# Performance work log

Measured on AMD Instinct MI355X. Metric: run time of the kernel, lower is better.

## Reference

```python
import jax, jax.numpy as jnp
import numpy as np

D_K = 64
TAU = 1.0
THRESHOLD = 0.5


def setup_inputs() -> dict:
    key = jax.random.key(0)
    k1, k2, k3 = jax.random.split(key, 3)
    B, N, F = 32, 512, 320
    F_OBS = 256
    h = jax.random.normal(k1, (B, N, F), dtype=jnp.float32)
    # xavier_uniform with gain 1.414 on (F_OBS, D_K)
    limit = float(1.414 * np.sqrt(6.0 / (F_OBS + D_K)))
    a_link = jax.random.uniform(k2, (F_OBS, D_K), minval=-limit, maxval=limit, dtype=jnp.float32)
    b_link = jax.random.uniform(k3, (F_OBS, D_K), minval=-limit, maxval=limit, dtype=jnp.float32)
    return {"h": h, "a_link": a_link, "b_link": b_link, "rollout": 1}


def reference(h, a_link, b_link, rollout):
    F_OBS = a_link.shape[0]
    # original detaches the sliced features
    hx = jax.lax.stop_gradient(h[:, :, :F_OBS])
    h_i = jnp.einsum('bik,kl->bil', hx, a_link)
    h_j = jnp.einsum('bjk,kl->bjl', hx, b_link)
    logits = jnp.einsum('bil,bjl->bij', h_i, h_j) / jnp.sqrt(jnp.float32(D_K))

    # gumbel_sigmoid with rollout=True: no noise, just sigmoid(logits/tau)
    y_soft = jax.nn.sigmoid(logits / TAU)
    y_hard = (y_soft > THRESHOLD).astype(y_soft.dtype)
    # straight-through estimator
    A = y_hard - jax.lax.stop_gradient(y_soft) + y_soft

    B, N, _ = logits.shape
    eye_b = jnp.eye(N, dtype=bool)[None]          # [1, N, N]
    eye_f = jnp.eye(N, dtype=y_soft.dtype)[None]  # [1, N, N]

    # log-prob of the sampled hard edges, off-diagonal entries only
    sel = A * y_soft + (1.0 - A) * (1.0 - y_soft)
    logp = jnp.log(sel + 1e-8)
    probs = jnp.sum(jnp.where(eye_b, 0.0, logp), axis=(1, 2))  # [B]

    # zero the diagonal of A, then add identity (vectorized form of the per-batch diag loop)
    A_out = A - A * eye_f + eye_f
    # .squeeze(0) is a no-op for B > 1
    return A_out, probs
```

## Files before the change

### kernel.cpp

```cpp
#include <hip/hip_runtime.h>
#include <math.h>

#define BATCH   32
#define NPTS    512
#define FDIM    320
#define FOBS    256
#define DK      64
#define MROWS   (BATCH * NPTS)
#define A_ELEMS ((size_t)BATCH * NPTS * NPTS)

typedef __bf16  bf16x8 __attribute__((ext_vector_type(8)));
typedef float   f32x4  __attribute__((ext_vector_type(4)));
typedef ushort  u16x8  __attribute__((ext_vector_type(8)));
typedef ushort  u16x4  __attribute__((ext_vector_type(4)));

__device__ __forceinline__ ushort f2bf(float f) {
    unsigned u = __builtin_bit_cast(unsigned, f);
    return (ushort)((u + 0x7fffu + ((u >> 16) & 1u)) >> 16);
}

__device__ __forceinline__ bf16x8 ld_bf8(const ushort* p) {
    return __builtin_bit_cast(bf16x8, *reinterpret_cast<const uint4*>(p));
}

__global__ __launch_bounds__(256) void k0_wt(const float* __restrict__ al,
                                             const float* __restrict__ bl,
                                             ushort* __restrict__ wt) {
    const int n = blockIdx.x;
    const int k = threadIdx.x;
    const float* src = (n < 64) ? al : bl;
    const int nn = n & 63;
    wt[(size_t)n * FOBS + k] = f2bf(src[(size_t)k * DK + nn]);
}

__global__ __launch_bounds__(256) void k1_mfma(const float* __restrict__ h,
                                               const ushort* __restrict__ wt,
                                               ushort* __restrict__ hi,
                                               ushort* __restrict__ hj) {
    const int t  = threadIdx.x;
    const int w  = t >> 6;
    const int l  = t & 63;
    const int lr = l & 15;
    const int lg = l >> 4;
    const int rb = blockIdx.x * 32 + 16 * (w & 1);
    const int cb = 64 * (w >> 1);

    const float* hrow = h + (size_t)(rb + lr) * FDIM;
    bf16x8 bfr[8];
#pragma unroll
    for (int ks = 0; ks < 8; ++ks) {
        const float* p = hrow + ks * 32 + lg * 8;
        float4 v0 = *reinterpret_cast<const float4*>(p);
        float4 v1 = *reinterpret_cast<const float4*>(p + 4);
        u16x8 u;
        u[0] = f2bf(v0.x); u[1] = f2bf(v0.y); u[2] = f2bf(v0.z); u[3] = f2bf(v0.w);
        u[4] = f2bf(v1.x); u[5] = f2bf(v1.y); u[6] = f2bf(v1.z); u[7] = f2bf(v1.w);
        bfr[ks] = __builtin_bit_cast(bf16x8, u);
    }

    f32x4 acc[4];
#pragma unroll
    for (int cf = 0; cf < 4; ++cf) acc[cf] = (f32x4){0.f, 0.f, 0.f, 0.f};

#pragma unroll
    for (int ks = 0; ks < 8; ++ks) {
#pragma unroll
        for (int cf = 0; cf < 4; ++cf) {
            bf16x8 afr = ld_bf8(&wt[(size_t)(cb + 16 * cf + lr) * FOBS + ks * 32 + lg * 8]);
            acc[cf] = __builtin_amdgcn_mfma_f32_16x16x32_bf16(afr, bfr[ks], acc[cf], 0, 0, 0);
        }
    }

    ushort* dst = (cb == 0) ? hi : hj;
    const size_t m = (size_t)(rb + lr);
#pragma unroll
    for (int cf = 0; cf < 4; ++cf) {
        u16x4 v;
#pragma unroll
        for (int r = 0; r < 4; ++r) v[r] = f2bf(acc[cf][r]);
        *reinterpret_cast<u16x4*>(&dst[m * DK + 16 * cf + lg * 4]) = v;
    }
}

__global__ __launch_bounds__(256, 4) void k2_mfma(const ushort* __restrict__ hi,
                                                  const ushort* __restrict__ hj,
                                                  float* __restrict__ Aout,
                                                  float* __restrict__ partials) {
    __shared__ float red[4];
    const int id  = blockIdx.x;
    const int sub = id >> 3;
    const int b   = (id & 7) * 4 + (sub >> 6);
    const int it  = (sub >> 3) & 7;
    const int jt  = sub & 7;

    const int t  = threadIdx.x;
    const int w  = t >> 6;
    const int l  = t & 63;
    const int lr = l & 15;
    const int lg = l >> 4;
    const int i0 = it * 64, j0 = jt * 64;

    const ushort* hib = hi + ((size_t)b * NPTS + i0) * DK;
    const ushort* hjb = hj + ((size_t)b * NPTS + j0) * DK;

    bf16x8 afr[2];
#pragma unroll
    for (int ks = 0; ks < 2; ++ks)
        afr[ks] = ld_bf8(&hjb[(size_t)(16 * w + lr) * DK + ks * 32 + lg * 8]);

    bf16x8 bfr[4][2];
#pragma unroll
    for (int itt = 0; itt < 4; ++itt)
#pragma unroll
        for (int ks = 0; ks < 2; ++ks)
            bfr[itt][ks] = ld_bf8(&hib[(size_t)(16 * itt + lr) * DK + ks * 32 + lg * 8]);

    f32x4 acc[4];
#pragma unroll
    for (int itt = 0; itt < 4; ++itt) acc[itt] = (f32x4){0.f, 0.f, 0.f, 0.f};

#pragma unroll
    for (int ks = 0; ks < 2; ++ks)
#pragma unroll
        for (int itt = 0; itt < 4; ++itt)
            acc[itt] = __builtin_amdgcn_mfma_f32_16x16x32_bf16(
                afr[ks], bfr[itt][ks], acc[itt], 0, 0, 0);

    float lsum = 0.f;
    const int colbase = j0 + 16 * w + lg * 4;
#pragma unroll
    for (int itt = 0; itt < 4; ++itt) {
        const int row = i0 + 16 * itt + lr;
        f32x4 ov;
#pragma unroll
        for (int r = 0; r < 4; ++r) {
            float x  = acc[itt][r] * 0.125f;
            float ax = fabsf(x);
            float nl = __logf(1.0f + __expf(-ax));
            bool diag = (row == colbase + r);
            ov[r] = (diag || x > 0.f) ? 1.f : 0.f;
            if (!diag) lsum -= nl;
        }
        __builtin_nontemporal_store(ov,
            reinterpret_cast<f32x4*>(&Aout[((size_t)b * NPTS + row) * NPTS + colbase]));
    }

#pragma unroll
    for (int off = 32; off > 0; off >>= 1) lsum += __shfl_down(lsum, off);
    if (l == 0) red[w] = lsum;
    __syncthreads();
    if (t == 0) {
        float s = (red[0] + red[1]) + (red[2] + red[3]);
        partials[(size_t)b * 64 + it * 8 + jt] = s;
    }
}

__global__ __launch_bounds__(64) void k3_reduce(const float* __restrict__ partials,
                                                float* __restrict__ probs) {
    int b = blockIdx.x;
    float s = partials[(size_t)b * 64 + threadIdx.x];
#pragma unroll
    for (int off = 32; off > 0; off >>= 1) s += __shfl_down(s, off);
    if (threadIdx.x == 0) probs[b] = s;
}

extern "C" void kernel_launch(void* const* d_in, const int* in_sizes, int n_in,
                              void* d_out, int out_size, void* d_ws, size_t ws_size,
                              hipStream_t stream) {
    const float* h  = (const float*)d_in[0];
    const float* al = (const float*)d_in[1];
    const float* bl = (const float*)d_in[2];
    float* out = (float*)d_out;

    ushort* hi      = (ushort*)d_ws;
    ushort* hj      = hi + (size_t)MROWS * DK;
    ushort* wt      = hj + (size_t)MROWS * DK;
    float* partials = (float*)(wt + 128 * FOBS);

    k0_wt<<<128, 256, 0, stream>>>(al, bl, wt);

    k1_mfma<<<MROWS / 32, 256, 0, stream>>>(h, wt, hi, hj);

    k2_mfma<<<(NPTS / 64) * (NPTS / 64) * BATCH, 256, 0, stream>>>(
        hi, hj, out, partials);

    k3_reduce<<<BATCH, 64, 0, stream>>>(partials, out + A_ELEMS);
}
```

Before: 38.70 us.

## Fuse projection GEMM into pairwise logits kernel, recompute h_j per tile

Merges the projection kernel and the pairwise logits kernel into one kernel. Each block computes its 64 h_i rows into swizzled LDS, then for four 64-column j tiles recomputes h_j from h and rearranges the accumulator fragments into MFMA operands with lane shuffles. This removes the hi/hj round trip through global memory and one launch. In exchange, h_j projection work is redundantly recomputed 8 times per batch, and the grid shrinks to 512 blocks.

```diff
diff --git a/kernel.cpp b/kernel.cpp
--- a/kernel.cpp
+++ b/kernel.cpp
@@ -11,16 +11,25 @@
 
 typedef __bf16  bf16x8 __attribute__((ext_vector_type(8)));
 typedef float   f32x4  __attribute__((ext_vector_type(4)));
-typedef ushort  u16x8  __attribute__((ext_vector_type(8)));
 typedef ushort  u16x4  __attribute__((ext_vector_type(4)));
 
 __device__ __forceinline__ ushort f2bf(float f) {
     unsigned u = __builtin_bit_cast(unsigned, f);
     return (ushort)((u + 0x7fffu + ((u >> 16) & 1u)) >> 16);
 }
-
+__device__ __forceinline__ unsigned pbf2(float a, float b) {
+    return (unsigned)f2bf(a) | ((unsigned)f2bf(b) << 16);
+}
 __device__ __forceinline__ bf16x8 ld_bf8(const ushort* p) {
     return __builtin_bit_cast(bf16x8, *reinterpret_cast<const uint4*>(p));
+}
+__device__ __forceinline__ bf16x8 cvt8(const float* p) {
+    float4 v0 = *reinterpret_cast<const float4*>(p);
+    float4 v1 = *reinterpret_cast<const float4*>(p + 4);
+    uint4 u;
+    u.x = pbf2(v0.x, v0.y); u.y = pbf2(v0.z, v0.w);
+    u.z = pbf2(v1.x, v1.y); u.w = pbf2(v1.z, v1.w);
+    return __builtin_bit_cast(bf16x8, u);
 }
 
 __global__ __launch_bounds__(256) void k0_wt(const float* __restrict__ al,
@@ -33,116 +42,139 @@
     wt[(size_t)n * FOBS + k] = f2bf(src[(size_t)k * DK + nn]);
 }
 
-__global__ __launch_bounds__(256) void k1_mfma(const float* __restrict__ h,
-                                               const ushort* __restrict__ wt,
-                                               ushort* __restrict__ hi,
-                                               ushort* __restrict__ hj) {
+__global__ __launch_bounds__(256, 3) void kU(const float* __restrict__ h,
+                                             const ushort* __restrict__ wt,
+                                             float* __restrict__ Aout,
+                                             float* __restrict__ partials) {
+    __shared__ ushort hi_lds[64][72];
+    __shared__ float red[4];
+
+    const int id  = blockIdx.x;
+    const int sub = id >> 3;
+    const int b   = (id & 7) * 4 + (sub >> 4);
+    const int rem = sub & 15;
+    const int it  = rem >> 1, jh = rem & 1;
+    const int i0 = it * 64, jbase = jh * 256;
+
     const int t  = threadIdx.x;
     const int w  = t >> 6;
     const int l  = t & 63;
     const int lr = l & 15;
     const int lg = l >> 4;
-    const int rb = blockIdx.x * 32 + 16 * (w & 1);
-    const int cb = 64 * (w >> 1);
-
-    const float* hrow = h + (size_t)(rb + lr) * FDIM;
-    bf16x8 bfr[8];
-#pragma unroll
-    for (int ks = 0; ks < 8; ++ks) {
-        const float* p = hrow + ks * 32 + lg * 8;
-        float4 v0 = *reinterpret_cast<const float4*>(p);
-        float4 v1 = *reinterpret_cast<const float4*>(p + 4);
-        u16x8 u;
-        u[0] = f2bf(v0.x); u[1] = f2bf(v0.y); u[2] = f2bf(v0.z); u[3] = f2bf(v0.w);
-        u[4] = f2bf(v1.x); u[5] = f2bf(v1.y); u[6] = f2bf(v1.z); u[7] = f2bf(v1.w);
-        bfr[ks] = __builtin_bit_cast(bf16x8, u);
+
+    const float* hb = h + (size_t)b * NPTS * FDIM;
+
+    {
+        const float* hrow = hb + (size_t)(i0 + 16 * w + lr) * FDIM;
+        bf16x8 hfr[8];
+#pragma unroll
+        for (int ks = 0; ks < 8; ++ks) hfr[ks] = cvt8(hrow + ks * 32 + lg * 8);
+
+        f32x4 acc[4];
+#pragma unroll
+        for (int cf = 0; cf < 4; ++cf) acc[cf] = (f32x4){0.f, 0.f, 0.f, 0.f};
+#pragma unroll
+        for (int ks = 0; ks < 8; ++ks)
+#pragma unroll
+            for (int cf = 0; cf < 4; ++cf) {
+                bf16x8 afr = ld_bf8(&wt[(size_t)(16 * cf + lr) * FOBS + ks * 32 + lg * 8]);
+                acc[cf] = __builtin_amdgcn_mfma_f32_16x16x32_bf16(afr, hfr[ks], acc[cf], 0, 0, 0);
+            }
+        const int row = 16 * w + lr;
+        const int xr  = (row & 3) << 4;
+#pragma unroll
+        for (int cf = 0; cf < 4; ++cf) {
+            u16x4 v;
+#pragma unroll
+            for (int r = 0; r < 4; ++r) v[r] = f2bf(acc[cf][r]);
+            int colb = (32 * cf + 8 * lg) ^ xr;
+            *reinterpret_cast<u16x4*>(reinterpret_cast<char*>(&hi_lds[row][0]) + colb) = v;
+        }
     }
-
-    f32x4 acc[4];
-#pragma unroll
-    for (int cf = 0; cf < 4; ++cf) acc[cf] = (f32x4){0.f, 0.f, 0.f, 0.f};
-
-#pragma unroll
-    for (int ks = 0; ks < 8; ++ks) {
+    __syncthreads();
+
+    bf16x8 hifr[4][2];
+#pragma unroll
+    for (int itt = 0; itt < 4; ++itt)
+#pragma unroll
+        for (int ks = 0; ks < 2; ++ks) {
+            int row  = 16 * itt + lr;
+            int colb = (64 * ks + 16 * lg) ^ ((row & 3) << 4);
+            hifr[itt][ks] = *reinterpret_cast<bf16x8*>(
+                reinterpret_cast<char*>(&hi_lds[row][0]) + colb);
+        }
+
+    float lsum = 0.f;
+    const int s0 = lr + 16 * (2 * (lg & 1));
+    const int s1 = s0 + 16;
+    const bool hicf = (lg >> 1) != 0;
+
+    for (int jt = 0; jt < 4; ++jt) {
+        const int j0 = jbase + jt * 64;
+
+        f32x4 acc[4];
+#pragma unroll
+        for (int cf = 0; cf < 4; ++cf) acc[cf] = (f32x4){0.f, 0.f, 0.f, 0.f};
+        {
+            const float* hrow = hb + (size_t)(j0 + 16 * w + lr) * FDIM;
+#pragma unroll
+            for (int ks = 0; ks < 8; ++ks) {
+                bf16x8 hfr = cvt8(hrow + ks * 32 + lg * 8);
+#pragma unroll
+                for (int cf = 0; cf < 4; ++cf) {
+                    bf16x8 afr = ld_bf8(&wt[(size_t)(64 + 16 * cf + lr) * FOBS + ks * 32 + lg * 8]);
+                    acc[cf] = __builtin_amdgcn_mfma_f32_16x16x32_bf16(afr, hfr, acc[cf], 0, 0, 0);
+                }
+            }
+        }
+        unsigned dA[4], dB[4];
 #pragma unroll
         for (int cf = 0; cf < 4; ++cf) {
-            bf16x8 afr = ld_bf8(&wt[(size_t)(cb + 16 * cf + lr) * FOBS + ks * 32 + lg * 8]);
-            acc[cf] = __builtin_amdgcn_mfma_f32_16x16x32_bf16(afr, bfr[ks], acc[cf], 0, 0, 0);
-        }
-    }
-
-    ushort* dst = (cb == 0) ? hi : hj;
-    const size_t m = (size_t)(rb + lr);
-#pragma unroll
-    for (int cf = 0; cf < 4; ++cf) {
-        u16x4 v;
-#pragma unroll
-        for (int r = 0; r < 4; ++r) v[r] = f2bf(acc[cf][r]);
-        *reinterpret_cast<u16x4*>(&dst[m * DK + 16 * cf + lg * 4]) = v;
-    }
-}
-
-__global__ __launch_bounds__(256, 4) void k2_mfma(const ushort* __restrict__ hi,
-                                                  const ushort* __restrict__ hj,
-                                                  float* __restrict__ Aout,
-                                                  float* __restrict__ partials) {
-    __shared__ float red[4];
-    const int id  = blockIdx.x;
-    const int sub = id >> 3;
-    const int b   = (id & 7) * 4 + (sub >> 6);
-    const int it  = (sub >> 3) & 7;
-    const int jt  = sub & 7;
-
-    const int t  = threadIdx.x;
-    const int w  = t >> 6;
-    const int l  = t & 63;
-    const int lr = l & 15;
-    const int lg = l >> 4;
-    const int i0 = it * 64, j0 = jt * 64;
-
-    const ushort* hib = hi + ((size_t)b * NPTS + i0) * DK;
-    const ushort* hjb = hj + ((size_t)b * NPTS + j0) * DK;
-
-    bf16x8 afr[2];
-#pragma unroll
-    for (int ks = 0; ks < 2; ++ks)
-        afr[ks] = ld_bf8(&hjb[(size_t)(16 * w + lr) * DK + ks * 32 + lg * 8]);
-
-    bf16x8 bfr[4][2];
-#pragma unroll
-    for (int itt = 0; itt < 4; ++itt)
+            dA[cf] = pbf2(acc[cf][0], acc[cf][1]);
+            dB[cf] = pbf2(acc[cf][2], acc[cf][3]);
+        }
+        bf16x8 ajf[2];
+#pragma unroll
+        for (int ks = 0; ks < 2; ++ks) {
+            unsigned d0a = __shfl(dA[2 * ks],     s0), d0b = __shfl(dA[2 * ks + 1], s0);
+            unsigned d1a = __shfl(dB[2 * ks],     s0), d1b = __shfl(dB[2 * ks + 1], s0);
+            unsigned d2a = __shfl(dA[2 * ks],     s1), d2b = __shfl(dA[2 * ks + 1], s1);
+            unsigned d3a = __shfl(dB[2 * ks],     s1), d3b = __shfl(dB[2 * ks + 1], s1);
+            uint4 u;
+            u.x = hicf ? d0b : d0a;
+            u.y = hicf ? d1b : d1a;
+            u.z = hicf ? d2b : d2a;
+            u.w = hicf ? d3b : d3a;
+            ajf[ks] = __builtin_bit_cast(bf16x8, u);
+        }
+
+        f32x4 lac[4];
+#pragma unroll
+        for (int itt = 0; itt < 4; ++itt) lac[itt] = (f32x4){0.f, 0.f, 0.f, 0.f};
 #pragma unroll
         for (int ks = 0; ks < 2; ++ks)
-            bfr[itt][ks] = ld_bf8(&hib[(size_t)(16 * itt + lr) * DK + ks * 32 + lg * 8]);
-
-    f32x4 acc[4];
-#pragma unroll
-    for (int itt = 0; itt < 4; ++itt) acc[itt] = (f32x4){0.f, 0.f, 0.f, 0.f};
-
-#pragma unroll
-    for (int ks = 0; ks < 2; ++ks)
-#pragma unroll
-        for (int itt = 0; itt < 4; ++itt)
-            acc[itt] = __builtin_amdgcn_mfma_f32_16x16x32_bf16(
-                afr[ks], bfr[itt][ks], acc[itt], 0, 0, 0);
-
-    float lsum = 0.f;
-    const int colbase = j0 + 16 * w + lg * 4;
-#pragma unroll
-    for (int itt = 0; itt < 4; ++itt) {
-        const int row = i0 + 16 * itt + lr;
-        f32x4 ov;
-#pragma unroll
-        for (int r = 0; r < 4; ++r) {
-            float x  = acc[itt][r] * 0.125f;
-            float ax = fabsf(x);
-            float nl = __logf(1.0f + __expf(-ax));
-            bool diag = (row == colbase + r);
-            ov[r] = (diag || x > 0.f) ? 1.f : 0.f;
-            if (!diag) lsum -= nl;
-        }
-        __builtin_nontemporal_store(ov,
-            reinterpret_cast<f32x4*>(&Aout[((size_t)b * NPTS + row) * NPTS + colbase]));
+#pragma unroll
+            for (int itt = 0; itt < 4; ++itt)
+                lac[itt] = __builtin_amdgcn_mfma_f32_16x16x32_bf16(
+                    ajf[ks], hifr[itt][ks], lac[itt], 0, 0, 0);
+
+        const int colbase = j0 + 16 * w + 4 * lg;
+#pragma unroll
+        for (int itt = 0; itt < 4; ++itt) {
+            const int row = i0 + 16 * itt + lr;
+            f32x4 ov;
+#pragma unroll
+            for (int r = 0; r < 4; ++r) {
+                float x  = lac[itt][r] * 0.125f;
+                float ax = fabsf(x);
+                float nl = __logf(1.0f + __expf(-ax));
+                bool diag = (row == colbase + r);
+                ov[r] = (diag || x > 0.f) ? 1.f : 0.f;
+                if (!diag) lsum -= nl;
+            }
+            __builtin_nontemporal_store(ov,
+                reinterpret_cast<f32x4*>(&Aout[((size_t)b * NPTS + row) * NPTS + colbase]));
+        }
     }
 
 #pragma unroll
@@ -151,14 +183,14 @@
     __syncthreads();
     if (t == 0) {
         float s = (red[0] + red[1]) + (red[2] + red[3]);
-        partials[(size_t)b * 64 + it * 8 + jt] = s;
+        partials[b * 16 + rem] = s;
     }
 }
 
 __global__ __launch_bounds__(64) void k3_reduce(const float* __restrict__ partials,
                                                 float* __restrict__ probs) {
     int b = blockIdx.x;
-    float s = partials[(size_t)b * 64 + threadIdx.x];
+    float s = (threadIdx.x < 16) ? partials[b * 16 + threadIdx.x] : 0.f;
 #pragma unroll
     for (int off = 32; off > 0; off >>= 1) s += __shfl_down(s, off);
     if (threadIdx.x == 0) probs[b] = s;
@@ -172,17 +204,12 @@
     const float* bl = (const float*)d_in[2];
     float* out = (float*)d_out;
 
-    ushort* hi      = (ushort*)d_ws;
-    ushort* hj      = hi + (size_t)MROWS * DK;
-    ushort* wt      = hj + (size_t)MROWS * DK;
+    ushort* wt      = (ushort*)d_ws;
     float* partials = (float*)(wt + 128 * FOBS);
 
     k0_wt<<<128, 256, 0, stream>>>(al, bl, wt);
 
-    k1_mfma<<<MROWS / 32, 256, 0, stream>>>(h, wt, hi, hj);
-
-    k2_mfma<<<(NPTS / 64) * (NPTS / 64) * BATCH, 256, 0, stream>>>(
-        hi, hj, out, partials);
+    kU<<<512, 256, 0, stream>>>(h, wt, out, partials);
 
     k3_reduce<<<BATCH, 64, 0, stream>>>(partials, out + A_ELEMS);
 }
```

Measured after the change: 63.76 us. 1.65x slower.

## Make k2 blocks loop over four j-tiles and split k1 across output columns

Applied to the files above, without the earlier changes.

The adjacency kernel now launches 512 blocks. Each block keeps its 64-row h_i fragments in registers and loops over four 64-column h_j tiles, instead of launching one block per 64x64 tile. This cuts redundant h_i loads and per-block launch and reduction overhead. It also leaves fewer blocks to hide the latency of the large output store stream, and partial sums drop to 16 per batch. The projection kernel now uses 16-row blocks with each wave computing 32 output columns, which doubles the block count and duplicates the h row loads across waves.

```diff
diff --git a/kernel.cpp b/kernel.cpp
--- a/kernel.cpp
+++ b/kernel.cpp
@@ -23,6 +23,15 @@
     return __builtin_bit_cast(bf16x8, *reinterpret_cast<const uint4*>(p));
 }
 
+__device__ __forceinline__ bf16x8 cvt8(const float* p) {
+    float4 v0 = *reinterpret_cast<const float4*>(p);
+    float4 v1 = *reinterpret_cast<const float4*>(p + 4);
+    u16x8 u;
+    u[0] = f2bf(v0.x); u[1] = f2bf(v0.y); u[2] = f2bf(v0.z); u[3] = f2bf(v0.w);
+    u[4] = f2bf(v1.x); u[5] = f2bf(v1.y); u[6] = f2bf(v1.z); u[7] = f2bf(v1.w);
+    return __builtin_bit_cast(bf16x8, u);
+}
+
 __global__ __launch_bounds__(256) void k0_wt(const float* __restrict__ al,
                                              const float* __restrict__ bl,
                                              ushort* __restrict__ wt) {
@@ -42,71 +51,60 @@
     const int l  = t & 63;
     const int lr = l & 15;
     const int lg = l >> 4;
-    const int rb = blockIdx.x * 32 + 16 * (w & 1);
-    const int cb = 64 * (w >> 1);
+    const int rb  = blockIdx.x * 16;
+    const int cbN = 32 * w;
 
     const float* hrow = h + (size_t)(rb + lr) * FDIM;
     bf16x8 bfr[8];
 #pragma unroll
-    for (int ks = 0; ks < 8; ++ks) {
-        const float* p = hrow + ks * 32 + lg * 8;
-        float4 v0 = *reinterpret_cast<const float4*>(p);
-        float4 v1 = *reinterpret_cast<const float4*>(p + 4);
-        u16x8 u;
-        u[0] = f2bf(v0.x); u[1] = f2bf(v0.y); u[2] = f2bf(v0.z); u[3] = f2bf(v0.w);
-        u[4] = f2bf(v1.x); u[5] = f2bf(v1.y); u[6] = f2bf(v1.z); u[7] = f2bf(v1.w);
-        bfr[ks] = __builtin_bit_cast(bf16x8, u);
-    }
+    for (int ks = 0; ks < 8; ++ks) bfr[ks] = cvt8(hrow + ks * 32 + lg * 8);
 
-    f32x4 acc[4];
+    f32x4 acc[2];
 #pragma unroll
-    for (int cf = 0; cf < 4; ++cf) acc[cf] = (f32x4){0.f, 0.f, 0.f, 0.f};
+    for (int cf = 0; cf < 2; ++cf) acc[cf] = (f32x4){0.f, 0.f, 0.f, 0.f};
 
 #pragma unroll
     for (int ks = 0; ks < 8; ++ks) {
 #pragma unroll
-        for (int cf = 0; cf < 4; ++cf) {
-            bf16x8 afr = ld_bf8(&wt[(size_t)(cb + 16 * cf + lr) * FOBS + ks * 32 + lg * 8]);
+        for (int cf = 0; cf < 2; ++cf) {
+            bf16x8 afr = ld_bf8(&wt[(size_t)(cbN + 16 * cf + lr) * FOBS + ks * 32 + lg * 8]);
             acc[cf] = __builtin_amdgcn_mfma_f32_16x16x32_bf16(afr, bfr[ks], acc[cf], 0, 0, 0);
         }
     }
 
-    ushort* dst = (cb == 0) ? hi : hj;
+    ushort* dst = (w >= 2) ? hj : hi;
+    const int nb = cbN & 63;
     const size_t m = (size_t)(rb + lr);
 #pragma unroll
-    for (int cf = 0; cf < 4; ++cf) {
+    for (int cf = 0; cf < 2; ++cf) {
         u16x4 v;
 #pragma unroll
         for (int r = 0; r < 4; ++r) v[r] = f2bf(acc[cf][r]);
-        *reinterpret_cast<u16x4*>(&dst[m * DK + 16 * cf + lg * 4]) = v;
+        *reinterpret_cast<u16x4*>(&dst[m * DK + nb + 16 * cf + 4 * lg]) = v;
     }
 }
 
-__global__ __launch_bounds__(256, 4) void k2_mfma(const ushort* __restrict__ hi,
-                                                  const ushort* __restrict__ hj,
-                                                  float* __restrict__ Aout,
-                                                  float* __restrict__ partials) {
+__global__ __launch_bounds__(256, 4) void k2fat(const ushort* __restrict__ hi,
+                                                const ushort* __restrict__ hj,
+                                                float* __restrict__ Aout,
+                                                float* __restrict__ partials) {
     __shared__ float red[4];
-    const int id  = blockIdx.x;
-    const int sub = id >> 3;
-    const int b   = (id & 7) * 4 + (sub >> 6);
-    const int it  = (sub >> 3) & 7;
-    const int jt  = sub & 7;
+    const int id = blockIdx.x;
+    const int b  = id >> 4;
+    const int it = (id >> 1) & 7;
+    const int jh = id & 1;
+    const int i0 = it * 64;
 
     const int t  = threadIdx.x;
     const int w  = t >> 6;
     const int l  = t & 63;
     const int lr = l & 15;
     const int lg = l >> 4;
-    const int i0 = it * 64, j0 = jt * 64;
 
-    const ushort* hib = hi + ((size_t)b * NPTS + i0) * DK;
-    const ushort* hjb = hj + ((size_t)b * NPTS + j0) * DK;
+    const ushort* hib  = hi + ((size_t)b * NPTS + i0) * DK;
+    const ushort* hjb0 = hj + ((size_t)b * NPTS + jh * 256) * DK;
 
-    bf16x8 afr[2];
-#pragma unroll
-    for (int ks = 0; ks < 2; ++ks)
-        afr[ks] = ld_bf8(&hjb[(size_t)(16 * w + lr) * DK + ks * 32 + lg * 8]);
+    float lsum = 0.f;
 
     bf16x8 bfr[4][2];
 #pragma unroll
@@ -115,34 +113,42 @@
         for (int ks = 0; ks < 2; ++ks)
             bfr[itt][ks] = ld_bf8(&hib[(size_t)(16 * itt + lr) * DK + ks * 32 + lg * 8]);
 
-    f32x4 acc[4];
+#pragma unroll 2
+    for (int jt2 = 0; jt2 < 4; ++jt2) {
+        const ushort* hjb = hjb0 + (size_t)jt2 * 64 * DK;
+        bf16x8 afr[2];
 #pragma unroll
-    for (int itt = 0; itt < 4; ++itt) acc[itt] = (f32x4){0.f, 0.f, 0.f, 0.f};
+        for (int ks = 0; ks < 2; ++ks)
+            afr[ks] = ld_bf8(&hjb[(size_t)(16 * w + lr) * DK + ks * 32 + lg * 8]);
 
+        f32x4 acc[4];
 #pragma unroll
-    for (int ks = 0; ks < 2; ++ks)
+        for (int itt = 0; itt < 4; ++itt) acc[itt] = (f32x4){0.f, 0.f, 0.f, 0.f};
 #pragma unroll
-        for (int itt = 0; itt < 4; ++itt)
-            acc[itt] = __builtin_amdgcn_mfma_f32_16x16x32_bf16(
-                afr[ks], bfr[itt][ks], acc[itt], 0, 0, 0);
+        for (int ks = 0; ks < 2; ++ks)
+#pragma unroll
+            for (int itt = 0; itt < 4; ++itt)
+                acc[itt] = __builtin_amdgcn_mfma_f32_16x16x32_bf16(
+                    afr[ks], bfr[itt][ks], acc[itt], 0, 0, 0);
 
-    float lsum = 0.f;
-    const int colbase = j0 + 16 * w + lg * 4;
+        const int j0 = jh * 256 + jt2 * 64;
+        const int colbase = j0 + 16 * w + 4 * lg;
 #pragma unroll
-    for (int itt = 0; itt < 4; ++itt) {
-        const int row = i0 + 16 * itt + lr;
-        f32x4 ov;
+        for (int itt = 0; itt < 4; ++itt) {
+            const int row = i0 + 16 * itt + lr;
+            f32x4 ov;
 #pragma unroll
-        for (int r = 0; r < 4; ++r) {
-            float x  = acc[itt][r] * 0.125f;
-            float ax = fabsf(x);
-            float nl = __logf(1.0f + __expf(-ax));
-            bool diag = (row == colbase + r);
-            ov[r] = (diag || x > 0.f) ? 1.f : 0.f;
-            if (!diag) lsum -= nl;
+            for (int r = 0; r < 4; ++r) {
+                float x  = acc[itt][r] * 0.125f;
+                float ax = fabsf(x);
+                float nl = __logf(1.0f + __expf(-ax));
+                bool diag = (row == colbase + r);
+                ov[r] = (diag || x > 0.f) ? 1.f : 0.f;
+                if (!diag) lsum -= nl;
+            }
+            __builtin_nontemporal_store(ov,
+                reinterpret_cast<f32x4*>(&Aout[((size_t)b * NPTS + row) * NPTS + colbase]));
         }
-        __builtin_nontemporal_store(ov,
-            reinterpret_cast<f32x4*>(&Aout[((size_t)b * NPTS + row) * NPTS + colbase]));
     }
 
 #pragma unroll
@@ -151,14 +157,14 @@
     __syncthreads();
     if (t == 0) {
         float s = (red[0] + red[1]) + (red[2] + red[3]);
-        partials[(size_t)b * 64 + it * 8 + jt] = s;
+        partials[id] = s;
     }
 }
 
 __global__ __launch_bounds__(64) void k3_reduce(const float* __restrict__ partials,
                                                 float* __restrict__ probs) {
     int b = blockIdx.x;
-    float s = partials[(size_t)b * 64 + threadIdx.x];
+    float s = (threadIdx.x < 16) ? partials[b * 16 + threadIdx.x] : 0.f;
 #pragma unroll
     for (int off = 32; off > 0; off >>= 1) s += __shfl_down(s, off);
     if (threadIdx.x == 0) probs[b] = s;
@@ -179,10 +185,9 @@
 
     k0_wt<<<128, 256, 0, stream>>>(al, bl, wt);
 
-    k1_mfma<<<MROWS / 32, 256, 0, stream>>>(h, wt, hi, hj);
+    k1_mfma<<<MROWS / 16, 256, 0, stream>>>(h, wt, hi, hj);
 
-    k2_mfma<<<(NPTS / 64) * (NPTS / 64) * BATCH, 256, 0, stream>>>(
-        hi, hj, out, partials);
+    k2fat<<<512, 256, 0, stream>>>(hi, hj, out, partials);
 
     k3_reduce<<<BATCH, 64, 0, stream>>>(partials, out + A_ELEMS);
 }
```

New measurement: 41.53 us. 1.07x slower.
